# Optimization experiments

Hardware: AMD Instinct MI355X
Metric: run time of the kernel (lower is better)

The kernel has to match this reference:

```python
import jax, jax.numpy as jnp
import numpy as np

NUM_HEADS = 16
HIDDEN = 1024
HEAD = HIDDEN // NUM_HEADS
SCALE = float(np.sqrt(HEAD))


def relu6(x):
    return jnp.minimum(jax.nn.relu(x), 6.0)


def setup_inputs() -> dict:
    key = jax.random.key(0)
    ks = jax.random.split(key, 9)
    T_t, T_s, B = 2048, 2048, 4
    init = 1.0 / np.sqrt(HIDDEN)  # torch Linear default uniform(-1/sqrt(fan_in), ...)
    return {
        "q": jax.random.normal(ks[0], (T_t, B, HIDDEN), jnp.float32),
        "k": jax.random.normal(ks[1], (T_s, B, HIDDEN), jnp.float32),
        "v": jax.random.normal(ks[2], (T_s, B, HIDDEN), jnp.float32),
        "Wq": jax.random.uniform(ks[3], (HIDDEN, HIDDEN), jnp.float32, -init, init),
        "bq": jax.random.uniform(ks[4], (HIDDEN,), jnp.float32, -init, init),
        "Wk": jax.random.uniform(ks[5], (HIDDEN, HIDDEN), jnp.float32, -init, init),
        "bk": jax.random.uniform(ks[6], (HIDDEN,), jnp.float32, -init, init),
        "Wv": jax.random.uniform(ks[7], (HIDDEN, HIDDEN), jnp.float32, -init, init),
        "bv": jax.random.uniform(ks[8], (HIDDEN,), jnp.float32, -init, init),
    }


def reference(q, k, v, Wq, bq, Wk, bk, Wv, bv):
    T_t, B, _ = q.shape
    T_s = k.shape[0]
    # QKV projections with ReLU6 (torch Linear: x @ W.T + b), then split heads
    qh = relu6(q @ Wq.T + bq).reshape(T_t, B, NUM_HEADS, HEAD)  # (T_t,B,h,d)
    kh = relu6(k @ Wk.T + bk).reshape(T_s, B, NUM_HEADS, HEAD)  # (T_s,B,h,d)
    vh = relu6(v @ Wv.T + bv).reshape(T_s, B, NUM_HEADS, HEAD)  # (T_s,B,h,d)
    # scores: (B,h,T_t,T_s)
    scores = jnp.einsum("tbhd,sbhd->bhts", qh, kh) / SCALE
    attn = jax.nn.softmax(scores, axis=-1)  # dropout is identity in eval mode
    out = jnp.einsum("bhts,sbhd->tbhd", attn, vh)  # (T_t,B,h,d)
    return out.reshape(T_t, B, NUM_HEADS * HEAD)
```

## Files before the change

### kernel.cpp

```cpp
#include <hip/hip_runtime.h>
#include <hip/hip_bf16.h>
#include <math.h>

#define HIDDEN 1024
#define NH 16
#define HD 64
#define TT 2048
#define NB 4
#define MROWS (TT*NB)
#define HEADSZ (TT*HD)

typedef __attribute__((ext_vector_type(8))) __bf16 bf16x8;
typedef __attribute__((ext_vector_type(2))) __bf16 bf16x2;
typedef __attribute__((ext_vector_type(8))) unsigned short u16x8;
typedef __attribute__((ext_vector_type(4))) float f32x4;
typedef __attribute__((ext_vector_type(4))) unsigned int u32x4;

__device__ __forceinline__ unsigned short f2bf(float x) {
  union { float f; unsigned int u; } v; v.f = x;
  unsigned int r = v.u + 0x7fffu + ((v.u >> 16) & 1u);
  return (unsigned short)(r >> 16);
}

__device__ __forceinline__ unsigned int packpair(float a, float b) {
#if __has_builtin(__builtin_amdgcn_cvt_pk_bf16_f32)
  bf16x2 t = __builtin_amdgcn_cvt_pk_bf16_f32(a, b);
  return __builtin_bit_cast(unsigned int, t);
#else
  return (unsigned int)f2bf(a) | ((unsigned int)f2bf(b) << 16);
#endif
}

__device__ __forceinline__ bf16x8 ld_frag(const unsigned short* p) {
  return __builtin_bit_cast(bf16x8, *(const u16x8*)p);
}

__device__ __forceinline__ void gload16(const void* g, void* l) {
  __builtin_amdgcn_global_load_lds(
      (const __attribute__((address_space(1))) void*)g,
      (__attribute__((address_space(3))) void*)l, 16, 0, 0);
}

__device__ __forceinline__ void stage32(const unsigned short* gp, unsigned short* lp) {
#pragma unroll
  for (int u = 0; u < 4; u++)
    *(u16x8*)(lp + u * 8) = *(const u16x8*)(gp + u * 8);
}
__device__ __forceinline__ void stage32(const float* gp, unsigned short* lp) {
#pragma unroll
  for (int u = 0; u < 4; u++) {
    float4 a0 = *(const float4*)(gp + u * 8);
    float4 a1 = *(const float4*)(gp + u * 8 + 4);
    u32x4 pk;
    pk.x = packpair(a0.x, a0.y); pk.y = packpair(a0.z, a0.w);
    pk.z = packpair(a1.x, a1.y); pk.w = packpair(a1.z, a1.w);
    *(u32x4*)(lp + u * 8) = pk;
  }
}

__global__ __launch_bounds__(256)
void cvt_kernel(const float* __restrict__ s, unsigned short* __restrict__ d, int n4) {
  int i = blockIdx.x * 256 + threadIdx.x;
  if (i >= n4) return;
  float4 f = ((const float4*)s)[i];
  unsigned int lo = packpair(f.x, f.y), hi = packpair(f.z, f.w);
  ((uint2*)d)[i] = make_uint2(lo, hi);
}

template<int VT>
__global__ __launch_bounds__(256)
void projg_kernel(const unsigned short* __restrict__ Xp, const unsigned short* __restrict__ Wp,
                  const float* __restrict__ bias, unsigned short* __restrict__ out)
{
  __shared__ __align__(16) unsigned short As[128 * 64];
  __shared__ __align__(16) unsigned short Bs[128 * 64];

  const int tid = threadIdx.x;
  const int lane = tid & 63;
  const int w = tid >> 6;
  const int wm = w & 1, wn = w >> 1;
  const int lr = lane & 15, lq = lane >> 4;
  const int bm = blockIdx.y, bn = blockIdx.x;

  const int srow = lane >> 3;
  const int schunk = (lane & 7) * 8;

  const unsigned short* Ag = Xp + (size_t)(bm * 128 + w * 32 + srow) * HIDDEN + schunk;
  const unsigned short* Bg = Wp + (size_t)(bn * 128 + w * 32 + srow) * HIDDEN + schunk;
  unsigned short* Al = &As[w * 32 * 64];
  unsigned short* Bl = &Bs[w * 32 * 64];

  f32x4 acc[4][4];
#pragma unroll
  for (int i = 0; i < 4; i++)
#pragma unroll
    for (int j = 0; j < 4; j++) acc[i][j] = (f32x4){0.f, 0.f, 0.f, 0.f};

  for (int k0 = 0; k0 < HIDDEN; k0 += 64) {
#pragma unroll
    for (int u = 0; u < 4; u++) {
      gload16(Ag + k0 + u * 8 * HIDDEN, Al + u * 512);
      gload16(Bg + k0 + u * 8 * HIDDEN, Bl + u * 512);
    }
    __syncthreads();
#pragma unroll
    for (int kk = 0; kk < 64; kk += 32) {
      bf16x8 af[4], bfr[4];
#pragma unroll
      for (int i = 0; i < 4; i++)
        af[i] = ld_frag(&As[(wm * 64 + i * 16 + lr) * 64 + kk + lq * 8]);
#pragma unroll
      for (int j = 0; j < 4; j++)
        bfr[j] = ld_frag(&Bs[(wn * 64 + j * 16 + lr) * 64 + kk + lq * 8]);
#pragma unroll
      for (int i = 0; i < 4; i++)
#pragma unroll
        for (int j = 0; j < 4; j++)
          acc[i][j] = __builtin_amdgcn_mfma_f32_16x16x32_bf16(af[i], bfr[j], acc[i][j], 0, 0, 0);
    }
    __syncthreads();
  }

#pragma unroll
  for (int j = 0; j < 4; j++) {
    const int n = bn * 128 + wn * 64 + j * 16 + lr;
    const float bb = bias[n];
    const int h = n >> 6, d = n & 63;
#pragma unroll
    for (int i = 0; i < 4; i++) {
      const int mb = bm * 128 + wm * 64 + i * 16 + lq * 4;
#pragma unroll
      for (int r = 0; r < 4; r++) {
        const int m = mb + r;
        const int t = m >> 2, b = m & 3;
        float vv = acc[i][j][r] + bb;
        vv = fminf(fmaxf(vv, 0.0f), 6.0f);
        if (VT) {
          const int s = t;
          const int st = s >> 7, sl = s & 127;
          const int a = (sl & 15) * 8 + (sl >> 4);
          out[(size_t)(b * NH + h) * HEADSZ + (size_t)d * TT + st * 128 + a] = f2bf(vv);
        } else {
          out[(size_t)(b * NH + h) * HEADSZ + (size_t)t * HD + d] = f2bf(vv);
        }
      }
    }
  }
}

#define PLD 72

template<int VT, typename XT, typename WT>
__global__ __launch_bounds__(256, 3)
void proj_kernel(const XT* __restrict__ Xp, const WT* __restrict__ Wp,
                 const float* __restrict__ bias, unsigned short* __restrict__ out)
{
  __shared__ unsigned short As[128 * PLD];
  __shared__ unsigned short Bs[128 * PLD];

  const int tid = threadIdx.x;
  const int lane = tid & 63;
  const int wid = tid >> 6;
  const int wm = wid & 1, wn = wid >> 1;
  const int lr = lane & 15, lq = lane >> 4;
  const int bm = blockIdx.y, bn = blockIdx.x;

  const int srow = tid >> 1;
  const int scol = (tid & 1) * 32;

  const XT* Ap = Xp + (size_t)(bm * 128 + srow) * HIDDEN + scol;
  const WT* Bp = Wp + (size_t)(bn * 128 + srow) * HIDDEN + scol;
  unsigned short* Asw = &As[srow * PLD + scol];
  unsigned short* Bsw = &Bs[srow * PLD + scol];

  f32x4 acc[4][4];
#pragma unroll
  for (int i = 0; i < 4; i++)
#pragma unroll
    for (int j = 0; j < 4; j++) acc[i][j] = (f32x4){0.f, 0.f, 0.f, 0.f};

  for (int k0 = 0; k0 < HIDDEN; k0 += 64) {
    stage32(Ap + k0, Asw);
    stage32(Bp + k0, Bsw);
    __syncthreads();
#pragma unroll
    for (int kk = 0; kk < 64; kk += 32) {
      bf16x8 af[4], bfr[4];
#pragma unroll
      for (int i = 0; i < 4; i++)
        af[i] = ld_frag(&As[(wm * 64 + i * 16 + lr) * PLD + kk + lq * 8]);
#pragma unroll
      for (int j = 0; j < 4; j++)
        bfr[j] = ld_frag(&Bs[(wn * 64 + j * 16 + lr) * PLD + kk + lq * 8]);
#pragma unroll
      for (int i = 0; i < 4; i++)
#pragma unroll
        for (int j = 0; j < 4; j++)
          acc[i][j] = __builtin_amdgcn_mfma_f32_16x16x32_bf16(af[i], bfr[j], acc[i][j], 0, 0, 0);
    }
    __syncthreads();
  }

#pragma unroll
  for (int j = 0; j < 4; j++) {
    const int n = bn * 128 + wn * 64 + j * 16 + lr;
    const float bb = bias[n];
    const int h = n >> 6, d = n & 63;
#pragma unroll
    for (int i = 0; i < 4; i++) {
      const int mb = bm * 128 + wm * 64 + i * 16 + lq * 4;
#pragma unroll
      for (int r = 0; r < 4; r++) {
        const int m = mb + r;
        const int t = m >> 2, b = m & 3;
        float vv = acc[i][j][r] + bb;
        vv = fminf(fmaxf(vv, 0.0f), 6.0f);
        if (VT) {
          const int s = t;
          const int st = s >> 7, sl = s & 127;
          const int a = (sl & 15) * 8 + (sl >> 4);
          out[(size_t)(b * NH + h) * HEADSZ + (size_t)d * TT + st * 128 + a] = f2bf(vv);
        } else {
          out[(size_t)(b * NH + h) * HEADSZ + (size_t)t * HD + d] = f2bf(vv);
        }
      }
    }
  }
}

#define QLD 72
#define PLDS 136
#define VLD 136
#define MBIAS 24.0f

__global__ __launch_bounds__(256, 3)
void attn_kernel(const unsigned short* __restrict__ qh,
                 const unsigned short* __restrict__ kh,
                 const unsigned short* __restrict__ vh,
                 float* __restrict__ outp)
{
  __shared__ unsigned short KPs[128 * PLDS];
  __shared__ unsigned short Vt[64 * VLD];

  const int tid = threadIdx.x;
  const int lane = tid & 63;
  const int w = tid >> 6;
  const int lr = lane & 15, lq = lane >> 4;
  const int qt = blockIdx.x, bh = blockIdx.y;
  const int b = bh >> 4, h = bh & 15;
  const int t0 = qt * 128;

  const size_t headoff = (size_t)bh * HEADSZ;

  {
    const unsigned short* qb = qh + headoff + (size_t)t0 * HD;
    const int row = tid >> 1, c0 = (tid & 1) * 32;
    stage32(qb + (size_t)row * HD + c0, &KPs[row * QLD + c0]);
  }
  __syncthreads();
  bf16x8 aq[2][2];
#pragma unroll
  for (int i = 0; i < 2; i++)
#pragma unroll
    for (int kx = 0; kx < 2; kx++)
      aq[i][kx] = ld_frag(&KPs[(w * 32 + i * 16 + lr) * QLD + kx * 32 + lq * 8]);
  __syncthreads();

  union { u16x8 v; unsigned short s[8]; } uo;
  const unsigned short ov = (lr == 0) ? (unsigned short)0x3F80 : (unsigned short)0;
#pragma unroll
  for (int z = 0; z < 8; z++) uo.s[z] = ov;
  const bf16x8 onesf = __builtin_bit_cast(bf16x8, uo.v);

  f32x4 Oacc[2][4];
  f32x4 lacc[2];
#pragma unroll
  for (int i = 0; i < 2; i++) {
#pragma unroll
    for (int jo = 0; jo < 4; jo++) Oacc[i][jo] = (f32x4){0.f, 0.f, 0.f, 0.f};
    lacc[i] = (f32x4){0.f, 0.f, 0.f, 0.f};
  }

  const float csc = 0.1803368801111204f;

  for (int st = 0; st < TT / 128; st++) {
    {
      const unsigned short* kb = kh + headoff + (size_t)st * (128 * HD);
      const int row = tid >> 1, c0 = (tid & 1) * 32;
      stage32(kb + (size_t)row * HD + c0, &KPs[row * QLD + c0]);
    }
    {
      const unsigned short* vb = vh + headoff + st * 128;
      const int dd = tid >> 2, a0 = (tid & 3) * 32;
#pragma unroll
      for (int u = 0; u < 4; u++)
        *(u16x8*)&Vt[dd * VLD + a0 + u * 8] = *(const u16x8*)(vb + (size_t)dd * TT + a0 + u * 8);
    }
    __syncthreads();

    f32x4 sc[2][8];
#pragma unroll
    for (int i = 0; i < 2; i++)
#pragma unroll
      for (int j = 0; j < 8; j++) sc[i][j] = (f32x4){0.f, 0.f, 0.f, 0.f};

#pragma unroll
    for (int kx = 0; kx < 2; kx++) {
#pragma unroll
      for (int j = 0; j < 8; j++) {
        bf16x8 bk = ld_frag(&KPs[(j * 16 + lr) * QLD + kx * 32 + lq * 8]);
#pragma unroll
        for (int i = 0; i < 2; i++)
          sc[i][j] = __builtin_amdgcn_mfma_f32_16x16x32_bf16(aq[i][kx], bk, sc[i][j], 0, 0, 0);
      }
    }
    __syncthreads();

#pragma unroll
    for (int i = 0; i < 2; i++)
#pragma unroll
      for (int j = 0; j < 8; j++)
#pragma unroll
        for (int r = 0; r < 4; r++)
          sc[i][j][r] = exp2f(fmaf(sc[i][j][r], csc, -MBIAS));

#pragma unroll
    for (int i = 0; i < 2; i++)
#pragma unroll
      for (int r = 0; r < 4; r++) {
        const int row = w * 32 + i * 16 + lq * 4 + r;
        u32x4 pk;
        pk.x = packpair(sc[i][0][r], sc[i][1][r]);
        pk.y = packpair(sc[i][2][r], sc[i][3][r]);
        pk.z = packpair(sc[i][4][r], sc[i][5][r]);
        pk.w = packpair(sc[i][6][r], sc[i][7][r]);
        *(u16x8*)&KPs[row * PLDS + lr * 8] = __builtin_bit_cast(u16x8, pk);
      }
    __syncthreads();

#pragma unroll
    for (int ks = 0; ks < 128; ks += 32) {
      bf16x8 ap[2];
#pragma unroll
      for (int i = 0; i < 2; i++)
        ap[i] = ld_frag(&KPs[(w * 32 + i * 16 + lr) * PLDS + ks + lq * 8]);
#pragma unroll
      for (int jo = 0; jo < 4; jo++) {
        bf16x8 bv2 = ld_frag(&Vt[(jo * 16 + lr) * VLD + ks + lq * 8]);
#pragma unroll
        for (int i = 0; i < 2; i++)
          Oacc[i][jo] = __builtin_amdgcn_mfma_f32_16x16x32_bf16(ap[i], bv2, Oacc[i][jo], 0, 0, 0);
      }
#pragma unroll
      for (int i = 0; i < 2; i++)
        lacc[i] = __builtin_amdgcn_mfma_f32_16x16x32_bf16(ap[i], onesf, lacc[i], 0, 0, 0);
    }
    __syncthreads();
  }

#pragma unroll
  for (int i = 0; i < 2; i++)
#pragma unroll
    for (int r = 0; r < 4; r++) {
      const float l = __shfl(lacc[i][r], lane & 48);
      const float inv = 1.0f / l;
      const int t = t0 + w * 32 + i * 16 + lq * 4 + r;
      float* op = outp + ((size_t)t * NB + b) * HIDDEN + h * HD;
#pragma unroll
      for (int jo = 0; jo < 4; jo++)
        op[jo * 16 + lr] = Oacc[i][jo][r] * inv;
    }
}

extern "C" void kernel_launch(void* const* d_in, const int* in_sizes, int n_in,
                              void* d_out, int out_size, void* d_ws, size_t ws_size,
                              hipStream_t stream)
{
  const float* q  = (const float*)d_in[0];
  const float* k  = (const float*)d_in[1];
  const float* v  = (const float*)d_in[2];
  const float* Wq = (const float*)d_in[3];
  const float* bq = (const float*)d_in[4];
  const float* Wk = (const float*)d_in[5];
  const float* bk = (const float*)d_in[6];
  const float* Wv = (const float*)d_in[7];
  const float* bv = (const float*)d_in[8];

  const size_t actN = (size_t)MROWS * HIDDEN;
  const size_t WN   = (size_t)HIDDEN * HIDDEN;
  unsigned short* qh  = (unsigned short*)d_ws;
  unsigned short* kh  = qh + actN;
  unsigned short* vh  = kh + actN;
  unsigned short* Wbf = vh + actN;
  unsigned short* Xbf = Wbf + WN;

  const size_t need_full = (3 * actN + WN + actN) * 2;
  const size_t need_w    = (3 * actN + WN) * 2;

  const int n4a = (int)(actN / 4);
  const int n4w = (int)(WN / 4);
  dim3 cga((n4a + 255) / 256), cgw((n4w + 255) / 256);
  dim3 pg(HIDDEN / 128, MROWS / 128);
  dim3 ag(TT / 128, NB * NH);

  if (ws_size >= need_full) {
    cvt_kernel<<<cga, 256, 0, stream>>>(q, Xbf, n4a);
    cvt_kernel<<<cgw, 256, 0, stream>>>(Wq, Wbf, n4w);
    projg_kernel<0><<<pg, 256, 0, stream>>>(Xbf, Wbf, bq, qh);
    cvt_kernel<<<cga, 256, 0, stream>>>(k, Xbf, n4a);
    cvt_kernel<<<cgw, 256, 0, stream>>>(Wk, Wbf, n4w);
    projg_kernel<0><<<pg, 256, 0, stream>>>(Xbf, Wbf, bk, kh);
    cvt_kernel<<<cga, 256, 0, stream>>>(v, Xbf, n4a);
    cvt_kernel<<<cgw, 256, 0, stream>>>(Wv, Wbf, n4w);
    projg_kernel<1><<<pg, 256, 0, stream>>>(Xbf, Wbf, bv, vh);
  } else if (ws_size >= need_w) {
    cvt_kernel<<<cgw, 256, 0, stream>>>(Wq, Wbf, n4w);
    proj_kernel<0, float, unsigned short><<<pg, 256, 0, stream>>>(q, Wbf, bq, qh);
    cvt_kernel<<<cgw, 256, 0, stream>>>(Wk, Wbf, n4w);
    proj_kernel<0, float, unsigned short><<<pg, 256, 0, stream>>>(k, Wbf, bk, kh);
    cvt_kernel<<<cgw, 256, 0, stream>>>(Wv, Wbf, n4w);
    proj_kernel<1, float, unsigned short><<<pg, 256, 0, stream>>>(v, Wbf, bv, vh);
  } else {
    proj_kernel<0, float, float><<<pg, 256, 0, stream>>>(q, Wq, bq, qh);
    proj_kernel<0, float, float><<<pg, 256, 0, stream>>>(k, Wk, bk, kh);
    proj_kernel<1, float, float><<<pg, 256, 0, stream>>>(v, Wv, bv, vh);
  }

  attn_kernel<<<ag, 256, 0, stream>>>(qh, kh, vh, (float*)d_out);
}
```

Baseline: 415.8 us.

## Fuse QKV projections into one launch and register-prefetch K/V tiles in attention

```diff
diff --git a/kernel.cpp b/kernel.cpp
--- a/kernel.cpp
+++ b/kernel.cpp
@@ -67,13 +67,36 @@
   ((uint2*)d)[i] = make_uint2(lo, hi);
 }
 
-template<int VT>
 __global__ __launch_bounds__(256)
-void projg_kernel(const unsigned short* __restrict__ Xp, const unsigned short* __restrict__ Wp,
-                  const float* __restrict__ bias, unsigned short* __restrict__ out)
+void cvtw_kernel(const float* __restrict__ a, const float* __restrict__ b,
+                 const float* __restrict__ c, unsigned short* __restrict__ d, int n4) {
+  const float* s = (blockIdx.y == 0) ? a : (blockIdx.y == 1) ? b : c;
+  int i = blockIdx.x * 256 + threadIdx.x;
+  if (i >= n4) return;
+  float4 f = ((const float4*)s)[i];
+  unsigned int lo = packpair(f.x, f.y), hi = packpair(f.z, f.w);
+  ((uint2*)(d + (size_t)blockIdx.y * (HIDDEN * HIDDEN)))[i] = make_uint2(lo, hi);
+}
+
+#define PLD 72
+
+__global__ __launch_bounds__(256, 3)
+void projf_kernel(const float* __restrict__ q, const float* __restrict__ k,
+                  const float* __restrict__ v,
+                  const unsigned short* __restrict__ Wb,
+                  const float* __restrict__ bq, const float* __restrict__ bk,
+                  const float* __restrict__ bv,
+                  unsigned short* __restrict__ outq, unsigned short* __restrict__ outk,
+                  unsigned short* __restrict__ outv)
 {
-  __shared__ __align__(16) unsigned short As[128 * 64];
+  __shared__ unsigned short As[128 * PLD];
   __shared__ __align__(16) unsigned short Bs[128 * 64];
+
+  const int z = blockIdx.z;
+  const float* Xp = (z == 0) ? q : (z == 1) ? k : v;
+  const unsigned short* Wp = Wb + (size_t)z * (HIDDEN * HIDDEN);
+  const float* bias = (z == 0) ? bq : (z == 1) ? bk : bv;
+  unsigned short* out = (z == 0) ? outq : (z == 1) ? outk : outv;
 
   const int tid = threadIdx.x;
   const int lane = tid & 63;
@@ -82,12 +105,12 @@
   const int lr = lane & 15, lq = lane >> 4;
   const int bm = blockIdx.y, bn = blockIdx.x;
 
-  const int srow = lane >> 3;
-  const int schunk = (lane & 7) * 8;
-
-  const unsigned short* Ag = Xp + (size_t)(bm * 128 + w * 32 + srow) * HIDDEN + schunk;
+  const int arow = tid >> 1, acol = (tid & 1) * 32;
+  const float* Ap = Xp + (size_t)(bm * 128 + arow) * HIDDEN + acol;
+  unsigned short* Asw = &As[arow * PLD + acol];
+
+  const int srow = lane >> 3, schunk = (lane & 7) * 8;
   const unsigned short* Bg = Wp + (size_t)(bn * 128 + w * 32 + srow) * HIDDEN + schunk;
-  unsigned short* Al = &As[w * 32 * 64];
   unsigned short* Bl = &Bs[w * 32 * 64];
 
   f32x4 acc[4][4];
@@ -98,20 +121,97 @@
 
   for (int k0 = 0; k0 < HIDDEN; k0 += 64) {
 #pragma unroll
-    for (int u = 0; u < 4; u++) {
-      gload16(Ag + k0 + u * 8 * HIDDEN, Al + u * 512);
+    for (int u = 0; u < 4; u++)
       gload16(Bg + k0 + u * 8 * HIDDEN, Bl + u * 512);
-    }
+    stage32(Ap + k0, Asw);
     __syncthreads();
 #pragma unroll
     for (int kk = 0; kk < 64; kk += 32) {
       bf16x8 af[4], bfr[4];
 #pragma unroll
       for (int i = 0; i < 4; i++)
-        af[i] = ld_frag(&As[(wm * 64 + i * 16 + lr) * 64 + kk + lq * 8]);
+        af[i] = ld_frag(&As[(wm * 64 + i * 16 + lr) * PLD + kk + lq * 8]);
 #pragma unroll
       for (int j = 0; j < 4; j++)
         bfr[j] = ld_frag(&Bs[(wn * 64 + j * 16 + lr) * 64 + kk + lq * 8]);
+#pragma unroll
+      for (int i = 0; i < 4; i++)
+#pragma unroll
+        for (int j = 0; j < 4; j++)
+          acc[i][j] = __builtin_amdgcn_mfma_f32_16x16x32_bf16(af[i], bfr[j], acc[i][j], 0, 0, 0);
+    }
+    __syncthreads();
+  }
+
+#pragma unroll
+  for (int j = 0; j < 4; j++) {
+    const int n = bn * 128 + wn * 64 + j * 16 + lr;
+    const float bb = bias[n];
+    const int h = n >> 6, d = n & 63;
+#pragma unroll
+    for (int i = 0; i < 4; i++) {
+      const int mb = bm * 128 + wm * 64 + i * 16 + lq * 4;
+#pragma unroll
+      for (int r = 0; r < 4; r++) {
+        const int m = mb + r;
+        const int t = m >> 2, b = m & 3;
+        float vv = acc[i][j][r] + bb;
+        vv = fminf(fmaxf(vv, 0.0f), 6.0f);
+        if (z == 2) {
+          const int s = t;
+          const int st = s >> 7, sl = s & 127;
+          const int a = (sl & 15) * 8 + (sl >> 4);
+          out[(size_t)(b * NH + h) * HEADSZ + (size_t)d * TT + st * 128 + a] = f2bf(vv);
+        } else {
+          out[(size_t)(b * NH + h) * HEADSZ + (size_t)t * HD + d] = f2bf(vv);
+        }
+      }
+    }
+  }
+}
+
+template<int VT, typename XT, typename WT>
+__global__ __launch_bounds__(256, 3)
+void proj_kernel(const XT* __restrict__ Xp, const WT* __restrict__ Wp,
+                 const float* __restrict__ bias, unsigned short* __restrict__ out)
+{
+  __shared__ unsigned short As[128 * PLD];
+  __shared__ unsigned short Bs[128 * PLD];
+
+  const int tid = threadIdx.x;
+  const int lane = tid & 63;
+  const int wid = tid >> 6;
+  const int wm = wid & 1, wn = wid >> 1;
+  const int lr = lane & 15, lq = lane >> 4;
+  const int bm = blockIdx.y, bn = blockIdx.x;
+
+  const int srow = tid >> 1;
+  const int scol = (tid & 1) * 32;
+
+  const XT* Ap = Xp + (size_t)(bm * 128 + srow) * HIDDEN + scol;
+  const WT* Bp = Wp + (size_t)(bn * 128 + srow) * HIDDEN + scol;
+  unsigned short* Asw = &As[srow * PLD + scol];
+  unsigned short* Bsw = &Bs[srow * PLD + scol];
+
+  f32x4 acc[4][4];
+#pragma unroll
+  for (int i = 0; i < 4; i++)
+#pragma unroll
+    for (int j = 0; j < 4; j++) acc[i][j] = (f32x4){0.f, 0.f, 0.f, 0.f};
+
+  for (int k0 = 0; k0 < HIDDEN; k0 += 64) {
+    stage32(Ap + k0, Asw);
+    stage32(Bp + k0, Bsw);
+    __syncthreads();
+#pragma unroll
+    for (int kk = 0; kk < 64; kk += 32) {
+      bf16x8 af[4], bfr[4];
+#pragma unroll
+      for (int i = 0; i < 4; i++)
+        af[i] = ld_frag(&As[(wm * 64 + i * 16 + lr) * PLD + kk + lq * 8]);
+#pragma unroll
+      for (int j = 0; j < 4; j++)
+        bfr[j] = ld_frag(&Bs[(wn * 64 + j * 16 + lr) * PLD + kk + lq * 8]);
 #pragma unroll
       for (int i = 0; i < 4; i++)
 #pragma unroll
@@ -148,86 +248,6 @@
   }
 }
 
-#define PLD 72
-
-template<int VT, typename XT, typename WT>
-__global__ __launch_bounds__(256, 3)
-void proj_kernel(const XT* __restrict__ Xp, const WT* __restrict__ Wp,
-                 const float* __restrict__ bias, unsigned short* __restrict__ out)
-{
-  __shared__ unsigned short As[128 * PLD];
-  __shared__ unsigned short Bs[128 * PLD];
-
-  const int tid = threadIdx.x;
-  const int lane = tid & 63;
-  const int wid = tid >> 6;
-  const int wm = wid & 1, wn = wid >> 1;
-  const int lr = lane & 15, lq = lane >> 4;
-  const int bm = blockIdx.y, bn = blockIdx.x;
-
-  const int srow = tid >> 1;
-  const int scol = (tid & 1) * 32;
-
-  const XT* Ap = Xp + (size_t)(bm * 128 + srow) * HIDDEN + scol;
-  const WT* Bp = Wp + (size_t)(bn * 128 + srow) * HIDDEN + scol;
-  unsigned short* Asw = &As[srow * PLD + scol];
-  unsigned short* Bsw = &Bs[srow * PLD + scol];
-
-  f32x4 acc[4][4];
-#pragma unroll
-  for (int i = 0; i < 4; i++)
-#pragma unroll
-    for (int j = 0; j < 4; j++) acc[i][j] = (f32x4){0.f, 0.f, 0.f, 0.f};
-
-  for (int k0 = 0; k0 < HIDDEN; k0 += 64) {
-    stage32(Ap + k0, Asw);
-    stage32(Bp + k0, Bsw);
-    __syncthreads();
-#pragma unroll
-    for (int kk = 0; kk < 64; kk += 32) {
-      bf16x8 af[4], bfr[4];
-#pragma unroll
-      for (int i = 0; i < 4; i++)
-        af[i] = ld_frag(&As[(wm * 64 + i * 16 + lr) * PLD + kk + lq * 8]);
-#pragma unroll
-      for (int j = 0; j < 4; j++)
-        bfr[j] = ld_frag(&Bs[(wn * 64 + j * 16 + lr) * PLD + kk + lq * 8]);
-#pragma unroll
-      for (int i = 0; i < 4; i++)
-#pragma unroll
-        for (int j = 0; j < 4; j++)
-          acc[i][j] = __builtin_amdgcn_mfma_f32_16x16x32_bf16(af[i], bfr[j], acc[i][j], 0, 0, 0);
-    }
-    __syncthreads();
-  }
-
-#pragma unroll
-  for (int j = 0; j < 4; j++) {
-    const int n = bn * 128 + wn * 64 + j * 16 + lr;
-    const float bb = bias[n];
-    const int h = n >> 6, d = n & 63;
-#pragma unroll
-    for (int i = 0; i < 4; i++) {
-      const int mb = bm * 128 + wm * 64 + i * 16 + lq * 4;
-#pragma unroll
-      for (int r = 0; r < 4; r++) {
-        const int m = mb + r;
-        const int t = m >> 2, b = m & 3;
-        float vv = acc[i][j][r] + bb;
-        vv = fminf(fmaxf(vv, 0.0f), 6.0f);
-        if (VT) {
-          const int s = t;
-          const int st = s >> 7, sl = s & 127;
-          const int a = (sl & 15) * 8 + (sl >> 4);
-          out[(size_t)(b * NH + h) * HEADSZ + (size_t)d * TT + st * 128 + a] = f2bf(vv);
-        } else {
-          out[(size_t)(b * NH + h) * HEADSZ + (size_t)t * HD + d] = f2bf(vv);
-        }
-      }
-    }
-  }
-}
-
 #define QLD 72
 #define PLDS 136
 #define VLD 136
@@ -252,11 +272,24 @@
 
   const size_t headoff = (size_t)bh * HEADSZ;
 
+  const int krow = tid >> 1, kc0 = (tid & 1) * 32;
+  const int vdd = tid >> 2, va0 = (tid & 3) * 32;
+  const unsigned short* kbase = kh + headoff + (size_t)krow * HD + kc0;
+  const unsigned short* vbase = vh + headoff + (size_t)vdd * TT + va0;
+  unsigned short* klds = &KPs[krow * QLD + kc0];
+  unsigned short* vlds = &Vt[vdd * VLD + va0];
+
   {
     const unsigned short* qb = qh + headoff + (size_t)t0 * HD;
-    const int row = tid >> 1, c0 = (tid & 1) * 32;
-    stage32(qb + (size_t)row * HD + c0, &KPs[row * QLD + c0]);
-  }
+    stage32(qb + (size_t)krow * HD + kc0, &KPs[krow * QLD + kc0]);
+  }
+
+  u16x8 kreg[4], vreg[4];
+#pragma unroll
+  for (int u = 0; u < 4; u++) kreg[u] = *(const u16x8*)(kbase + u * 8);
+#pragma unroll
+  for (int u = 0; u < 4; u++) vreg[u] = *(const u16x8*)(vbase + u * 8);
+
   __syncthreads();
   bf16x8 aq[2][2];
 #pragma unroll
@@ -284,19 +317,20 @@
   const float csc = 0.1803368801111204f;
 
   for (int st = 0; st < TT / 128; st++) {
-    {
-      const unsigned short* kb = kh + headoff + (size_t)st * (128 * HD);
-      const int row = tid >> 1, c0 = (tid & 1) * 32;
-      stage32(kb + (size_t)row * HD + c0, &KPs[row * QLD + c0]);
-    }
-    {
-      const unsigned short* vb = vh + headoff + st * 128;
-      const int dd = tid >> 2, a0 = (tid & 3) * 32;
-#pragma unroll
-      for (int u = 0; u < 4; u++)
-        *(u16x8*)&Vt[dd * VLD + a0 + u * 8] = *(const u16x8*)(vb + (size_t)dd * TT + a0 + u * 8);
-    }
-    __syncthreads();
+#pragma unroll
+    for (int u = 0; u < 4; u++) *(u16x8*)(klds + u * 8) = kreg[u];
+#pragma unroll
+    for (int u = 0; u < 4; u++) *(u16x8*)(vlds + u * 8) = vreg[u];
+    __syncthreads();
+
+    if (st + 1 < TT / 128) {
+      const unsigned short* kn = kbase + (size_t)(st + 1) * (128 * HD);
+      const unsigned short* vn = vbase + (size_t)(st + 1) * 128;
+#pragma unroll
+      for (int u = 0; u < 4; u++) kreg[u] = *(const u16x8*)(kn + u * 8);
+#pragma unroll
+      for (int u = 0; u < 4; u++) vreg[u] = *(const u16x8*)(vn + u * 8);
+    }
 
     f32x4 sc[2][8];
 #pragma unroll
@@ -304,6 +338,7 @@
 #pragma unroll
       for (int j = 0; j < 8; j++) sc[i][j] = (f32x4){0.f, 0.f, 0.f, 0.f};
 
+    __builtin_amdgcn_s_setprio(1);
 #pragma unroll
     for (int kx = 0; kx < 2; kx++) {
 #pragma unroll
@@ -314,6 +349,7 @@
           sc[i][j] = __builtin_amdgcn_mfma_f32_16x16x32_bf16(aq[i][kx], bk, sc[i][j], 0, 0, 0);
       }
     }
+    __builtin_amdgcn_s_setprio(0);
     __syncthreads();
 
 #pragma unroll
@@ -338,6 +374,7 @@
       }
     __syncthreads();
 
+    __builtin_amdgcn_s_setprio(1);
 #pragma unroll
     for (int ks = 0; ks < 128; ks += 32) {
       bf16x8 ap[2];
@@ -355,6 +392,7 @@
       for (int i = 0; i < 2; i++)
         lacc[i] = __builtin_amdgcn_mfma_f32_16x16x32_bf16(ap[i], onesf, lacc[i], 0, 0, 0);
     }
+    __builtin_amdgcn_s_setprio(0);
     __syncthreads();
   }
 
@@ -391,29 +429,23 @@
   unsigned short* qh  = (unsigned short*)d_ws;
   unsigned short* kh  = qh + actN;
   unsigned short* vh  = kh + actN;
-  unsigned short* Wbf = vh + actN;
-  unsigned short* Xbf = Wbf + WN;
-
-  const size_t need_full = (3 * actN + WN + actN) * 2;
-  const size_t need_w    = (3 * actN + WN) * 2;
-
-  const int n4a = (int)(actN / 4);
+  unsigned short* Wb3 = vh + actN;
+
+  const size_t need_fused = (3 * actN + 3 * WN) * 2;
+  const size_t need_w     = (3 * actN + WN) * 2;
+
   const int n4w = (int)(WN / 4);
-  dim3 cga((n4a + 255) / 256), cgw((n4w + 255) / 256);
+  dim3 cgw((n4w + 255) / 256);
   dim3 pg(HIDDEN / 128, MROWS / 128);
+  dim3 pf(HIDDEN / 128, MROWS / 128, 3);
   dim3 ag(TT / 128, NB * NH);
 
-  if (ws_size >= need_full) {
-    cvt_kernel<<<cga, 256, 0, stream>>>(q, Xbf, n4a);
-    cvt_kernel<<<cgw, 256, 0, stream>>>(Wq, Wbf, n4w);
-    projg_kernel<0><<<pg, 256, 0, stream>>>(Xbf, Wbf, bq, qh);
-    cvt_kernel<<<cga, 256, 0, stream>>>(k, Xbf, n4a);
-    cvt_kernel<<<cgw, 256, 0, stream>>>(Wk, Wbf, n4w);
-    projg_kernel<0><<<pg, 256, 0, stream>>>(Xbf, Wbf, bk, kh);
-    cvt_kernel<<<cga, 256, 0, stream>>>(v, Xbf, n4a);
-    cvt_kernel<<<cgw, 256, 0, stream>>>(Wv, Wbf, n4w);
-    projg_kernel<1><<<pg, 256, 0, stream>>>(Xbf, Wbf, bv, vh);
+  if (ws_size >= need_fused) {
+    dim3 cw((n4w + 255) / 256, 3);
+    cvtw_kernel<<<cw, 256, 0, stream>>>(Wq, Wk, Wv, Wb3, n4w);
+    projf_kernel<<<pf, 256, 0, stream>>>(q, k, v, Wb3, bq, bk, bv, qh, kh, vh);
   } else if (ws_size >= need_w) {
+    unsigned short* Wbf = vh + actN;
     cvt_kernel<<<cgw, 256, 0, stream>>>(Wq, Wbf, n4w);
     proj_kernel<0, float, unsigned short><<<pg, 256, 0, stream>>>(q, Wbf, bq, qh);
     cvt_kernel<<<cgw, 256, 0, stream>>>(Wk, Wbf, n4w);
```

New measurement: 482.6 us. +16.1%, slower.

## Batch Q/K/V conversion and projection into single launches; add MFMA priority hints

Applied to the files above, without the earlier changes.

```diff
diff --git a/kernel.cpp b/kernel.cpp
--- a/kernel.cpp
+++ b/kernel.cpp
@@ -65,6 +65,108 @@
   float4 f = ((const float4*)s)[i];
   unsigned int lo = packpair(f.x, f.y), hi = packpair(f.z, f.w);
   ((uint2*)d)[i] = make_uint2(lo, hi);
+}
+
+__global__ __launch_bounds__(256)
+void cvt3_kernel(const float* __restrict__ a, const float* __restrict__ b,
+                 const float* __restrict__ c, unsigned short* __restrict__ d,
+                 int n4, long long stride4) {
+  const float* s = (blockIdx.y == 0) ? a : (blockIdx.y == 1) ? b : c;
+  int i = blockIdx.x * 256 + threadIdx.x;
+  if (i >= n4) return;
+  float4 f = ((const float4*)s)[i];
+  unsigned int lo = packpair(f.x, f.y), hi = packpair(f.z, f.w);
+  ((uint2*)d)[(size_t)blockIdx.y * stride4 + i] = make_uint2(lo, hi);
+}
+
+__global__ __launch_bounds__(256)
+void projg3_kernel(const unsigned short* __restrict__ Xb,
+                   const unsigned short* __restrict__ Wb,
+                   const float* __restrict__ bq, const float* __restrict__ bk,
+                   const float* __restrict__ bv,
+                   unsigned short* __restrict__ outq, unsigned short* __restrict__ outk,
+                   unsigned short* __restrict__ outv)
+{
+  __shared__ __align__(16) unsigned short As[128 * 64];
+  __shared__ __align__(16) unsigned short Bs[128 * 64];
+
+  const int z = blockIdx.z;
+  const unsigned short* Xp = Xb + (size_t)z * ((size_t)MROWS * HIDDEN);
+  const unsigned short* Wp = Wb + (size_t)z * ((size_t)HIDDEN * HIDDEN);
+  const float* bias = (z == 0) ? bq : (z == 1) ? bk : bv;
+  unsigned short* out = (z == 0) ? outq : (z == 1) ? outk : outv;
+
+  const int tid = threadIdx.x;
+  const int lane = tid & 63;
+  const int w = tid >> 6;
+  const int wm = w & 1, wn = w >> 1;
+  const int lr = lane & 15, lq = lane >> 4;
+  const int bm = blockIdx.y, bn = blockIdx.x;
+
+  const int srow = lane >> 3;
+  const int schunk = (lane & 7) * 8;
+
+  const unsigned short* Ag = Xp + (size_t)(bm * 128 + w * 32 + srow) * HIDDEN + schunk;
+  const unsigned short* Bg = Wp + (size_t)(bn * 128 + w * 32 + srow) * HIDDEN + schunk;
+  unsigned short* Al = &As[w * 32 * 64];
+  unsigned short* Bl = &Bs[w * 32 * 64];
+
+  f32x4 acc[4][4];
+#pragma unroll
+  for (int i = 0; i < 4; i++)
+#pragma unroll
+    for (int j = 0; j < 4; j++) acc[i][j] = (f32x4){0.f, 0.f, 0.f, 0.f};
+
+  for (int k0 = 0; k0 < HIDDEN; k0 += 64) {
+#pragma unroll
+    for (int u = 0; u < 4; u++) {
+      gload16(Ag + k0 + u * 8 * HIDDEN, Al + u * 512);
+      gload16(Bg + k0 + u * 8 * HIDDEN, Bl + u * 512);
+    }
+    __syncthreads();
+#pragma unroll
+    for (int kk = 0; kk < 64; kk += 32) {
+      bf16x8 af[4], bfr[4];
+#pragma unroll
+      for (int i = 0; i < 4; i++)
+        af[i] = ld_frag(&As[(wm * 64 + i * 16 + lr) * 64 + kk + lq * 8]);
+#pragma unroll
+      for (int j = 0; j < 4; j++)
+        bfr[j] = ld_frag(&Bs[(wn * 64 + j * 16 + lr) * 64 + kk + lq * 8]);
+#pragma unroll
+      for (int i = 0; i < 4; i++)
+#pragma unroll
+        for (int j = 0; j < 4; j++)
+          acc[i][j] = __builtin_amdgcn_mfma_f32_16x16x32_bf16(af[i], bfr[j], acc[i][j], 0, 0, 0);
+    }
+    __syncthreads();
+  }
+
+#pragma unroll
+  for (int j = 0; j < 4; j++) {
+    const int n = bn * 128 + wn * 64 + j * 16 + lr;
+    const float bb = bias[n];
+    const int h = n >> 6, d = n & 63;
+#pragma unroll
+    for (int i = 0; i < 4; i++) {
+      const int mb = bm * 128 + wm * 64 + i * 16 + lq * 4;
+#pragma unroll
+      for (int r = 0; r < 4; r++) {
+        const int m = mb + r;
+        const int t = m >> 2, b = m & 3;
+        float vv = acc[i][j][r] + bb;
+        vv = fminf(fmaxf(vv, 0.0f), 6.0f);
+        if (z == 2) {
+          const int s = t;
+          const int st = s >> 7, sl = s & 127;
+          const int a = (sl & 15) * 8 + (sl >> 4);
+          out[(size_t)(b * NH + h) * HEADSZ + (size_t)d * TT + st * 128 + a] = f2bf(vv);
+        } else {
+          out[(size_t)(b * NH + h) * HEADSZ + (size_t)t * HD + d] = f2bf(vv);
+        }
+      }
+    }
+  }
 }
 
 template<int VT>
@@ -304,6 +406,7 @@
 #pragma unroll
       for (int j = 0; j < 8; j++) sc[i][j] = (f32x4){0.f, 0.f, 0.f, 0.f};
 
+    __builtin_amdgcn_s_setprio(1);
 #pragma unroll
     for (int kx = 0; kx < 2; kx++) {
 #pragma unroll
@@ -314,6 +417,7 @@
           sc[i][j] = __builtin_amdgcn_mfma_f32_16x16x32_bf16(aq[i][kx], bk, sc[i][j], 0, 0, 0);
       }
     }
+    __builtin_amdgcn_s_setprio(0);
     __syncthreads();
 
 #pragma unroll
@@ -338,6 +442,7 @@
       }
     __syncthreads();
 
+    __builtin_amdgcn_s_setprio(1);
 #pragma unroll
     for (int ks = 0; ks < 128; ks += 32) {
       bf16x8 ap[2];
@@ -355,6 +460,7 @@
       for (int i = 0; i < 2; i++)
         lacc[i] = __builtin_amdgcn_mfma_f32_16x16x32_bf16(ap[i], onesf, lacc[i], 0, 0, 0);
     }
+    __builtin_amdgcn_s_setprio(0);
     __syncthreads();
   }
 
@@ -391,19 +497,28 @@
   unsigned short* qh  = (unsigned short*)d_ws;
   unsigned short* kh  = qh + actN;
   unsigned short* vh  = kh + actN;
-  unsigned short* Wbf = vh + actN;
-  unsigned short* Xbf = Wbf + WN;
-
-  const size_t need_full = (3 * actN + WN + actN) * 2;
-  const size_t need_w    = (3 * actN + WN) * 2;
+  unsigned short* Wb3 = vh + actN;
+  unsigned short* Xb3 = Wb3 + 3 * WN;
+
+  const size_t need_fused = (6 * actN + 3 * WN) * 2;
+  const size_t need_full  = (4 * actN + WN) * 2;
+  const size_t need_w     = (3 * actN + WN) * 2;
 
   const int n4a = (int)(actN / 4);
   const int n4w = (int)(WN / 4);
   dim3 cga((n4a + 255) / 256), cgw((n4w + 255) / 256);
   dim3 pg(HIDDEN / 128, MROWS / 128);
+  dim3 pf(HIDDEN / 128, MROWS / 128, 3);
   dim3 ag(TT / 128, NB * NH);
 
-  if (ws_size >= need_full) {
+  if (ws_size >= need_fused) {
+    dim3 cw(cgw.x, 3), cx(cga.x, 3);
+    cvt3_kernel<<<cw, 256, 0, stream>>>(Wq, Wk, Wv, Wb3, n4w, (long long)(WN / 4));
+    cvt3_kernel<<<cx, 256, 0, stream>>>(q, k, v, Xb3, n4a, (long long)(actN / 4));
+    projg3_kernel<<<pf, 256, 0, stream>>>(Xb3, Wb3, bq, bk, bv, qh, kh, vh);
+  } else if (ws_size >= need_full) {
+    unsigned short* Wbf = vh + actN;
+    unsigned short* Xbf = Wbf + WN;
     cvt_kernel<<<cga, 256, 0, stream>>>(q, Xbf, n4a);
     cvt_kernel<<<cgw, 256, 0, stream>>>(Wq, Wbf, n4w);
     projg_kernel<0><<<pg, 256, 0, stream>>>(Xbf, Wbf, bq, qh);
@@ -414,6 +529,7 @@
     cvt_kernel<<<cgw, 256, 0, stream>>>(Wv, Wbf, n4w);
     projg_kernel<1><<<pg, 256, 0, stream>>>(Xbf, Wbf, bv, vh);
   } else if (ws_size >= need_w) {
+    unsigned short* Wbf = vh + actN;
     cvt_kernel<<<cgw, 256, 0, stream>>>(Wq, Wbf, n4w);
     proj_kernel<0, float, unsigned short><<<pg, 256, 0, stream>>>(q, Wbf, bq, qh);
     cvt_kernel<<<cgw, 256, 0, stream>>>(Wk, Wbf, n4w);
```

Measured after the change: 387.7 us. 1.07x faster.
